# Performance work log

Hardware: AMD Instinct MI355X
Metric: run time of the kernel (lower is better)

The kernel has to match this reference:

```python
import jax, jax.numpy as jnp
import numpy as np

N_NODES = 100000
N_EDGES = 1600000
IN_CH = 128
OUT_CH = 64
HID = 2 * OUT_CH  # 128


def setup_inputs() -> dict:
    key = jax.random.key(0)
    ks = jax.random.split(key, 8)
    s = lambda fan_in: 1.0 / np.sqrt(fan_in)
    return {
        "x": jax.random.normal(ks[0], (N_NODES, IN_CH), jnp.float32),
        "edge_index": jax.random.randint(ks[1], (2, N_EDGES), 0, N_NODES, dtype=jnp.int32),
        "W1": jax.random.normal(ks[2], (IN_CH, HID), jnp.float32) * s(IN_CH),
        "b1": jnp.zeros((HID,), jnp.float32),
        "W2": jax.random.normal(ks[3], (HID, HID), jnp.float32) * s(HID),
        "b2": jnp.zeros((HID,), jnp.float32),
        "W3": jax.random.normal(ks[4], (HID, OUT_CH), jnp.float32) * s(HID),
        "b3": jnp.zeros((OUT_CH,), jnp.float32),
    }


def reference(x, edge_index, W1, b1, W2, b2, W3, b3):
    N = x.shape[0]
    # GCNConv (PyG semantics): add self-loops, symmetric deg^{-1/2} normalization,
    # linear transform, scatter-add aggregation at destination, then bias.
    loops = jnp.arange(N, dtype=edge_index.dtype)
    src = jnp.concatenate([edge_index[0], loops])  # [E+N]
    dst = jnp.concatenate([edge_index[1], loops])  # [E+N]
    deg = jnp.zeros((N,), x.dtype).at[dst].add(1.0)  # in-degree incl. self-loop
    dinv = jnp.where(deg > 0, jax.lax.rsqrt(deg), 0.0)
    norm = (dinv[src] * dinv[dst])[:, None]  # [E+N, 1]

    def gcn_conv(h, W, b):
        h = h @ W  # transform first (smaller when out < in)
        msg = h[src] * norm  # gather + normalize, [E+N, C]
        agg = jnp.zeros((N, h.shape[1]), h.dtype).at[dst].add(msg)  # scatter-add
        return agg + b

    h = jax.nn.relu(gcn_conv(x, W1, b1))
    h = jax.nn.relu(gcn_conv(h, W2, b2))
    h = gcn_conv(h, W3, b3)
    return jnp.min(h, axis=0)  # min-pool over nodes -> [OUT_CH]
```

## Files before the change

### kernel.cpp

```cpp
#include <hip/hip_runtime.h>
#include <stdint.h>
#include <stddef.h>
#include <float.h>

typedef short bf16x8 __attribute__((ext_vector_type(8)));
typedef float f32x4 __attribute__((ext_vector_type(4)));

static __device__ __forceinline__ unsigned enc_min(float v) {
  unsigned u = __float_as_uint(v);
  return (u & 0x80000000u) ? ~u : (u | 0x80000000u);
}
static __device__ __forceinline__ unsigned short f2bf(float f) {
  unsigned u = __float_as_uint(f);
  u += 0x7fffu + ((u >> 16) & 1u);
  return (unsigned short)(u >> 16);
}
static __device__ __forceinline__ float bf2f(unsigned short b) {
  return __uint_as_float(((unsigned)b) << 16);
}
static __device__ __forceinline__ void acc8(float* a, uint4 v) {
  a[0] += __uint_as_float(v.x << 16);
  a[1] += __uint_as_float(v.x & 0xffff0000u);
  a[2] += __uint_as_float(v.y << 16);
  a[3] += __uint_as_float(v.y & 0xffff0000u);
  a[4] += __uint_as_float(v.z << 16);
  a[5] += __uint_as_float(v.z & 0xffff0000u);
  a[6] += __uint_as_float(v.w << 16);
  a[7] += __uint_as_float(v.w & 0xffff0000u);
}

__global__ __launch_bounds__(256) void k_count_bin(const int* __restrict__ edge, int E, int N,
                                                   int* __restrict__ cnt8,
                                                   int* __restrict__ bin_cur,
                                                   int2* __restrict__ pairs,
                                                   int binw, int bcap) {
  __shared__ int h[8], gbase[8], lfill[8];
  int cslot = blockIdx.x & 7;
  int* cnt = cnt8 + (size_t)cslot * N;
  int tid = threadIdx.x;
  int nt = (E + 1023) >> 10;
  for (int t = blockIdx.x; t < nt; t += gridDim.x) {
    int e0 = t << 10;
    if (tid < 8) { h[tid] = 0; lfill[tid] = 0; }
    __syncthreads();
    int d[4], s[4], g[4], r[4];
#pragma unroll
    for (int k = 0; k < 4; ++k) {
      int e = e0 + tid + k * 256;
      d[k] = -1;
      if (e < E) {
        d[k] = edge[E + e];
        s[k] = edge[e];
        g[k] = (int)((unsigned)d[k] / (unsigned)binw);
        r[k] = atomicAdd(&cnt[d[k]], 1);
        atomicAdd(&h[g[k]], 1);
      }
    }
    __syncthreads();
    if (tid < 8) gbase[tid] = atomicAdd(&bin_cur[tid], h[tid]);
    __syncthreads();
#pragma unroll
    for (int k = 0; k < 4; ++k) {
      if (d[k] >= 0) {
        int rr = atomicAdd(&lfill[g[k]], 1);
        int p = gbase[g[k]] + rr;
        unsigned packed = (unsigned)d[k] | ((unsigned)cslot << 17) | ((unsigned)r[k] << 20);
        if (p < bcap) pairs[(size_t)g[k] * bcap + p] = make_int2((int)packed, s[k]);
      }
    }
    __syncthreads();
  }
}

__global__ void k_scan1(const int* __restrict__ cnt8, int N,
                        int* __restrict__ cnt, int* __restrict__ incl,
                        int* __restrict__ bsum) {
  __shared__ int sm[1024];
  int tid = threadIdx.x;
  int i = blockIdx.x * 1024 + tid;
  int v = 0;
  if (i < N) {
#pragma unroll
    for (int g = 0; g < 8; ++g) v += cnt8[(size_t)g * N + i];
    cnt[i] = v;
  }
  sm[tid] = v;
  __syncthreads();
  for (int off = 1; off < 1024; off <<= 1) {
    int t = (tid >= off) ? sm[tid - off] : 0;
    __syncthreads();
    sm[tid] += t;
    __syncthreads();
  }
  if (i < N) incl[i] = sm[tid];
  if (tid == 1023) bsum[blockIdx.x] = sm[1023];
}

__global__ void k_scan2(const int* __restrict__ bsum, int nb, int* __restrict__ boff) {
  __shared__ int sm[128];
  int tid = threadIdx.x;
  int v = (tid < nb) ? bsum[tid] : 0;
  sm[tid] = v;
  __syncthreads();
  for (int off = 1; off < 128; off <<= 1) {
    int t = (tid >= off) ? sm[tid - off] : 0;
    __syncthreads();
    sm[tid] += t;
    __syncthreads();
  }
  if (tid < nb) boff[tid] = sm[tid] - v;
}

__global__ void k_aux(const int* __restrict__ cnt, const int* __restrict__ cnt8,
                      const int* __restrict__ incl, const int* __restrict__ boff,
                      int N, int E, int* __restrict__ row_ptr,
                      int* __restrict__ base8, float* __restrict__ dinv) {
  int i = blockIdx.x * blockDim.x + threadIdx.x;
  if (i < N) {
    int rp = incl[i] - cnt[i] + boff[i >> 10];
    row_ptr[i] = rp;
    dinv[i] = 1.0f / sqrtf((float)(cnt[i] + 1));
    int run = rp;
#pragma unroll
    for (int c = 0; c < 8; ++c) {
      base8[(size_t)c * N + i] = run;
      run += cnt8[(size_t)c * N + i];
    }
  } else if (i == N) {
    row_ptr[N] = E;
  }
}

__global__ void k_prepw(const float* __restrict__ W1, const float* __restrict__ W2,
                        const float* __restrict__ W3,
                        unsigned short* __restrict__ w1h, unsigned short* __restrict__ w1l,
                        unsigned short* __restrict__ w2h, unsigned short* __restrict__ w2l,
                        unsigned short* __restrict__ w3h, unsigned short* __restrict__ w3l) {
  const int K = 128;
  int idx = blockIdx.x * 256 + threadIdx.x;
  const float* W;
  unsigned short *oh, *ol;
  int Nn, base;
  if (idx < 16384) { W = W1; Nn = 128; oh = w1h; ol = w1l; base = idx; }
  else if (idx < 32768) { W = W2; Nn = 128; oh = w2h; ol = w2l; base = idx - 16384; }
  else if (idx < 40960) { W = W3; Nn = 64; oh = w3h; ol = w3l; base = idx - 32768; }
  else return;
  int n = base / K, k = base % K;
  float w = W[(size_t)k * Nn + n];
  unsigned short h = f2bf(w);
  unsigned short l = f2bf(w - bf2f(h));
  int nf = n >> 4, mloc = n & 15, kci = k >> 5, quad = (k >> 3) & 3, j = k & 7;
  size_t o = ((size_t)((nf * 4 + kci) * 64 + quad * 16 + mloc)) * 8 + j;
  oh[o] = h;
  ol[o] = l;
}

template <int NFW>
static __device__ __forceinline__ void gemm_body(const float* __restrict__ A,
                                                 const unsigned short* __restrict__ Wfh,
                                                 const unsigned short* __restrict__ Wfl,
                                                 const float* __restrict__ dinv,
                                                 unsigned short* __restrict__ P, int M,
                                                 int blk) {
  const int K = 128;
  const int COUT = NFW * 64;
  __shared__ unsigned short Ah[64][136];
  __shared__ unsigned short Al[64][136];
  int tid = threadIdx.x;
  int m0 = blk * 64;
  int w = tid >> 6, lane = tid & 63;

  bf16x8 bh[NFW][4], bl[NFW][4];
#pragma unroll
  for (int i = 0; i < NFW; ++i)
#pragma unroll
    for (int kci = 0; kci < 4; ++kci) {
      size_t o = ((size_t)(((w * NFW + i) * 4 + kci) * 64 + lane)) * 8;
      bh[i][kci] = *(const bf16x8*)&Wfh[o];
      bl[i][kci] = *(const bf16x8*)&Wfl[o];
    }

#pragma unroll
  for (int q = 0; q < 8; ++q) {
    int f = q * 256 + tid;
    int m = f >> 5, k4 = f & 31;
    int row = m0 + m;
    if (row >= M) row = M - 1;
    float4 v = *(const float4*)&A[(size_t)row * K + k4 * 4];
    unsigned short h0 = f2bf(v.x), h1 = f2bf(v.y), h2 = f2bf(v.z), h3 = f2bf(v.w);
    unsigned short l0 = f2bf(v.x - bf2f(h0)), l1 = f2bf(v.y - bf2f(h1));
    unsigned short l2 = f2bf(v.z - bf2f(h2)), l3 = f2bf(v.w - bf2f(h3));
    uint2 hh, ll;
    hh.x = (unsigned)h0 | ((unsigned)h1 << 16);
    hh.y = (unsigned)h2 | ((unsigned)h3 << 16);
    ll.x = (unsigned)l0 | ((unsigned)l1 << 16);
    ll.y = (unsigned)l2 | ((unsigned)l3 << 16);
    *(uint2*)&Ah[m][k4 * 4] = hh;
    *(uint2*)&Al[m][k4 * 4] = ll;
  }
  __syncthreads();

  int mloc = lane & 15, quad = lane >> 4;
  f32x4 acc[4][NFW];
#pragma unroll
  for (int rt = 0; rt < 4; ++rt)
#pragma unroll
    for (int i = 0; i < NFW; ++i) acc[rt][i] = (f32x4){0.f, 0.f, 0.f, 0.f};

#pragma unroll
  for (int rt = 0; rt < 4; ++rt) {
    const unsigned short* ph = &Ah[rt * 16 + mloc][quad * 8];
    const unsigned short* pl = &Al[rt * 16 + mloc][quad * 8];
#pragma unroll
    for (int kci = 0; kci < 4; ++kci) {
      bf16x8 ah = *(const bf16x8*)(ph + kci * 32);
      bf16x8 al = *(const bf16x8*)(pl + kci * 32);
#pragma unroll
      for (int i = 0; i < NFW; ++i) {
        acc[rt][i] = __builtin_amdgcn_mfma_f32_16x16x32_bf16(al, bh[i][kci], acc[rt][i], 0, 0, 0);
        acc[rt][i] = __builtin_amdgcn_mfma_f32_16x16x32_bf16(ah, bl[i][kci], acc[rt][i], 0, 0, 0);
        acc[rt][i] = __builtin_amdgcn_mfma_f32_16x16x32_bf16(ah, bh[i][kci], acc[rt][i], 0, 0, 0);
      }
    }
  }

#pragma unroll
  for (int rt = 0; rt < 4; ++rt) {
    int rbase = m0 + rt * 16 + quad * 4;
#pragma unroll
    for (int r = 0; r < 4; ++r) {
      int row = rbase + r;
      if (row < M) {
        float dv = dinv[row];
#pragma unroll
        for (int i = 0; i < NFW; ++i) {
          int nf = w * NFW + i;
          P[(size_t)row * COUT + nf * 16 + mloc] = f2bf(acc[rt][i][r] * dv);
        }
      }
    }
  }
}

__global__ __launch_bounds__(256) void k_fill_gemm(const float* __restrict__ A,
                                                   const unsigned short* __restrict__ Wfh,
                                                   const unsigned short* __restrict__ Wfl,
                                                   const float* __restrict__ dinv,
                                                   unsigned short* __restrict__ P, int M,
                                                   const int2* __restrict__ pairs,
                                                   const int* __restrict__ bin_cur, int bcap,
                                                   const int* __restrict__ base8, int N,
                                                   int* __restrict__ srcs, int ns) {
  if ((int)blockIdx.x >= ns) {
    gemm_body<2>(A, Wfh, Wfl, dinv, P, M, blockIdx.x - ns);
  } else {
    int grp = blockIdx.x & 7;
    int bslot = blockIdx.x >> 3;
    int nslot = ns >> 3;
    int cnt_g = bin_cur[grp];
    if (cnt_g > bcap) cnt_g = bcap;
    const int2* pp = pairs + (size_t)grp * bcap;
    for (int i = bslot * blockDim.x + threadIdx.x; i < cnt_g; i += nslot * blockDim.x) {
      int2 pr = pp[i];
      unsigned w = (unsigned)pr.x;
      int d = (int)(w & 0x1FFFFu);
      int c = (int)((w >> 17) & 7u);
      int r = (int)(w >> 20);
      srcs[base8[(size_t)c * N + d] + r] = pr.y;
    }
  }
}

template <int NFW>
__global__ __launch_bounds__(256) void k_agg_gemm(const unsigned short* __restrict__ Pin,
                                                  const int* __restrict__ row_ptr,
                                                  const int* __restrict__ srcs,
                                                  const float* __restrict__ dinv,
                                                  const float* __restrict__ bias,
                                                  const unsigned short* __restrict__ Wfh,
                                                  const unsigned short* __restrict__ Wfl,
                                                  unsigned short* __restrict__ Pout, int N) {
  const int COUT = NFW * 64;
  __shared__ unsigned short Ah[16][136];
  __shared__ unsigned short Al[16][136];
  int tid = threadIdx.x;
  int wv = tid >> 6, lane = tid & 63;
  int grp = lane >> 4, sub = lane & 15;
  int m = wv * 4 + grp;
  int d = blockIdx.x * 16 + m;
  int dc = d < N ? d : N - 1;
  bool valid = d < N;
  unsigned soff = (unsigned)sub * 16u;
  const char* Pb = (const char*)Pin;

  float a[8] = {0.f, 0.f, 0.f, 0.f, 0.f, 0.f, 0.f, 0.f};
  {
    uint4 v = *(const uint4*)(Pb + ((unsigned)dc * 256u + soff));
    acc8(a, v);
  }
  int lo = row_ptr[dc];
  int hi = row_ptr[valid ? d + 1 : dc];
  int j = lo;
  for (; j + 8 <= hi; j += 8) {
    unsigned id[8];
    uint4 vv[8];
#pragma unroll
    for (int k = 0; k < 8; ++k) id[k] = (unsigned)srcs[j + k];
#pragma unroll
    for (int k = 0; k < 8; ++k) vv[k] = *(const uint4*)(Pb + (id[k] * 256u + soff));
#pragma unroll
    for (int k = 0; k < 8; ++k) acc8(a, vv[k]);
  }
  for (; j + 4 <= hi; j += 4) {
    unsigned id[4];
    uint4 vv[4];
#pragma unroll
    for (int k = 0; k < 4; ++k) id[k] = (unsigned)srcs[j + k];
#pragma unroll
    for (int k = 0; k < 4; ++k) vv[k] = *(const uint4*)(Pb + (id[k] * 256u + soff));
#pragma unroll
    for (int k = 0; k < 4; ++k) acc8(a, vv[k]);
  }
  for (; j < hi; ++j) {
    unsigned i0 = (unsigned)srcs[j];
    uint4 v0 = *(const uint4*)(Pb + (i0 * 256u + soff));
    acc8(a, v0);
  }

  bf16x8 bh[NFW][4], bl[NFW][4];
#pragma unroll
  for (int i = 0; i < NFW; ++i)
#pragma unroll
    for (int kci = 0; kci < 4; ++kci) {
      size_t o = ((size_t)(((wv * NFW + i) * 4 + kci) * 64 + lane)) * 8;
      bh[i][kci] = *(const bf16x8*)&Wfh[o];
      bl[i][kci] = *(const bf16x8*)&Wfl[o];
    }

  float dv = dinv[dc];
  int ch0 = sub * 8;
  float4 bv0 = *(const float4*)&bias[ch0];
  float4 bv1 = *(const float4*)&bias[ch0 + 4];
  float h[8];
  h[0] = dv * a[0] + bv0.x; h[1] = dv * a[1] + bv0.y;
  h[2] = dv * a[2] + bv0.z; h[3] = dv * a[3] + bv0.w;
  h[4] = dv * a[4] + bv1.x; h[5] = dv * a[5] + bv1.y;
  h[6] = dv * a[6] + bv1.z; h[7] = dv * a[7] + bv1.w;
#pragma unroll
  for (int k = 0; k < 8; ++k) h[k] = fmaxf(h[k], 0.f);
  unsigned short hb[8], lb[8];
#pragma unroll
  for (int k = 0; k < 8; ++k) {
    hb[k] = f2bf(h[k]);
    lb[k] = f2bf(h[k] - bf2f(hb[k]));
  }
  uint4 HH, LL;
  HH.x = (unsigned)hb[0] | ((unsigned)hb[1] << 16);
  HH.y = (unsigned)hb[2] | ((unsigned)hb[3] << 16);
  HH.z = (unsigned)hb[4] | ((unsigned)hb[5] << 16);
  HH.w = (unsigned)hb[6] | ((unsigned)hb[7] << 16);
  LL.x = (unsigned)lb[0] | ((unsigned)lb[1] << 16);
  LL.y = (unsigned)lb[2] | ((unsigned)lb[3] << 16);
  LL.z = (unsigned)lb[4] | ((unsigned)lb[5] << 16);
  LL.w = (unsigned)lb[6] | ((unsigned)lb[7] << 16);
  *(uint4*)&Ah[m][ch0] = HH;
  *(uint4*)&Al[m][ch0] = LL;
  __syncthreads();

  int mloc = lane & 15, quad = lane >> 4;
  f32x4 acc[NFW];
#pragma unroll
  for (int i = 0; i < NFW; ++i) acc[i] = (f32x4){0.f, 0.f, 0.f, 0.f};
#pragma unroll
  for (int kci = 0; kci < 4; ++kci) {
    bf16x8 ah = *(const bf16x8*)&Ah[mloc][quad * 8 + kci * 32];
    bf16x8 al = *(const bf16x8*)&Al[mloc][quad * 8 + kci * 32];
#pragma unroll
    for (int i = 0; i < NFW; ++i) {
      acc[i] = __builtin_amdgcn_mfma_f32_16x16x32_bf16(al, bh[i][kci], acc[i], 0, 0, 0);
      acc[i] = __builtin_amdgcn_mfma_f32_16x16x32_bf16(ah, bl[i][kci], acc[i], 0, 0, 0);
      acc[i] = __builtin_amdgcn_mfma_f32_16x16x32_bf16(ah, bh[i][kci], acc[i], 0, 0, 0);
    }
  }
  int rbase = blockIdx.x * 16 + quad * 4;
#pragma unroll
  for (int r = 0; r < 4; ++r) {
    int row = rbase + r;
    if (row < N) {
      float dvr = dinv[row];
#pragma unroll
      for (int i = 0; i < NFW; ++i) {
        int nf = wv * NFW + i;
        Pout[(size_t)row * COUT + nf * 16 + mloc] = f2bf(acc[i][r] * dvr);
      }
    }
  }
}

__global__ __launch_bounds__(256) void k_agg_pool(const unsigned short* __restrict__ P,
                                                  const int* __restrict__ row_ptr,
                                                  const int* __restrict__ srcs,
                                                  const float* __restrict__ dinv,
                                                  const float* __restrict__ bias,
                                                  unsigned* __restrict__ minenc, int N) {
  __shared__ float s_red[4][64];
  int tid = threadIdx.x;
  int wv = tid >> 6, lane = tid & 63;
  int g = lane >> 3, q = lane & 7;
  int d = blockIdx.x * 32 + wv * 8 + g;
  bool valid = d < N;
  int dc = valid ? d : N - 1;
  const char* Pb = (const char*)P;
  unsigned soff = (unsigned)q * 16u;

  float a[8] = {0.f, 0.f, 0.f, 0.f, 0.f, 0.f, 0.f, 0.f};
  {
    uint4 v = *(const uint4*)(Pb + ((unsigned)dc * 128u + soff));
    acc8(a, v);
  }
  int lo = row_ptr[dc];
  int hi = row_ptr[valid ? d + 1 : dc];
  int j = lo;
  for (; j + 8 <= hi; j += 8) {
    unsigned id[8];
    uint4 vv[8];
#pragma unroll
    for (int k = 0; k < 8; ++k) id[k] = (unsigned)srcs[j + k];
#pragma unroll
    for (int k = 0; k < 8; ++k) vv[k] = *(const uint4*)(Pb + (id[k] * 128u + soff));
#pragma unroll
    for (int k = 0; k < 8; ++k) acc8(a, vv[k]);
  }
  for (; j < hi; ++j) {
    unsigned i0 = (unsigned)srcs[j];
    uint4 v0 = *(const uint4*)(Pb + (i0 * 128u + soff));
    acc8(a, v0);
  }

  float dv = dinv[dc];
  int c0 = q * 8;
  float4 bv0 = *(const float4*)&bias[c0];
  float4 bv1 = *(const float4*)&bias[c0 + 4];
  float h[8];
  h[0] = dv * a[0] + bv0.x; h[1] = dv * a[1] + bv0.y;
  h[2] = dv * a[2] + bv0.z; h[3] = dv * a[3] + bv0.w;
  h[4] = dv * a[4] + bv1.x; h[5] = dv * a[5] + bv1.y;
  h[6] = dv * a[6] + bv1.z; h[7] = dv * a[7] + bv1.w;
  if (!valid) {
#pragma unroll
    for (int k = 0; k < 8; ++k) h[k] = FLT_MAX;
  }
#pragma unroll
  for (int off = 8; off < 64; off <<= 1) {
#pragma unroll
    for (int k = 0; k < 8; ++k) h[k] = fminf(h[k], __shfl_xor(h[k], off, 64));
  }
  if (lane < 8) {
#pragma unroll
    for (int k = 0; k < 8; ++k) s_red[wv][q * 8 + k] = h[k];
  }
  __syncthreads();
  if (tid < 64) {
    float mn = fminf(fminf(s_red[0][tid], s_red[1][tid]),
                     fminf(s_red[2][tid], s_red[3][tid]));
    atomicMin(&minenc[tid], enc_min(mn));
  }
}

__global__ void k_decode(const unsigned* __restrict__ minenc, float* __restrict__ out) {
  int c = threadIdx.x;
  unsigned k = minenc[c];
  unsigned u = (k & 0x80000000u) ? (k & 0x7FFFFFFFu) : ~k;
  out[c] = __uint_as_float(u);
}

extern "C" void kernel_launch(void* const* d_in, const int* in_sizes, int n_in,
                              void* d_out, int out_size, void* d_ws, size_t ws_size,
                              hipStream_t stream) {
  const float* X  = (const float*)d_in[0];
  const int* edge = (const int*)d_in[1];
  const float* W1 = (const float*)d_in[2];
  const float* b1 = (const float*)d_in[3];
  const float* W2 = (const float*)d_in[4];
  const float* b2 = (const float*)d_in[5];
  const float* W3 = (const float*)d_in[6];
  const float* b3 = (const float*)d_in[7];
  float* out = (float*)d_out;

  const int IN_CH = 128;
  int N = in_sizes[0] / IN_CH;
  int E = in_sizes[1] / 2;

  char* ws = (char*)d_ws;
  size_t off = 0;
  auto alloc = [&](size_t bytes) {
    void* p = ws + off;
    off = (off + bytes + 255) & ~(size_t)255;
    return p;
  };
  unsigned short* P1 = (unsigned short*)alloc((size_t)N * 128 * 2);
  unsigned short* P2 = (unsigned short*)alloc((size_t)N * 128 * 2);
  int* srcs      = (int*)alloc((size_t)E * 4);
  int* cnt8      = (int*)alloc((size_t)8 * N * 4);
  int* base8     = (int*)alloc((size_t)8 * N * 4);
  int* cnt       = (int*)alloc((size_t)N * 4);
  int* incl      = (int*)alloc((size_t)N * 4);
  int* row_ptr   = (int*)alloc((size_t)(N + 1) * 4);
  float* dinv    = (float*)alloc((size_t)N * 4);
  int* bsum      = (int*)alloc(1024);
  int* boff      = (int*)alloc(1024);
  int* bin_cur   = (int*)alloc(256);
  unsigned* minenc = (unsigned*)alloc(256);
  unsigned short* w1h = (unsigned short*)alloc(16384 * 2);
  unsigned short* w1l = (unsigned short*)alloc(16384 * 2);
  unsigned short* w2h = (unsigned short*)alloc(16384 * 2);
  unsigned short* w2l = (unsigned short*)alloc(16384 * 2);
  unsigned short* w3h = (unsigned short*)alloc(8192 * 2);
  unsigned short* w3l = (unsigned short*)alloc(8192 * 2);

  int bcap = E / 8 + 65536;
  int binw = (N + 7) / 8;
  int2* pairs = (int2*)P2;
  unsigned short* P3 = P1;

  hipMemsetAsync(cnt8, 0, (size_t)8 * N * 4, stream);
  hipMemsetAsync(bin_cur, 0, 32, stream);
  hipMemsetAsync(minenc, 0xFF, 64 * 4, stream);

  int nb = (N + 1023) / 1024;
  int gx = (N + 63) / 64;
  int ns = 1024;
  int gagg = (N + 15) / 16;
  int gpool = (N + 31) / 32;
  k_prepw<<<160, 256, 0, stream>>>(W1, W2, W3, w1h, w1l, w2h, w2l, w3h, w3l);
  k_count_bin<<<782, 256, 0, stream>>>(edge, E, N, cnt8, bin_cur, pairs, binw, bcap);
  k_scan1<<<nb, 1024, 0, stream>>>(cnt8, N, cnt, incl, bsum);
  k_scan2<<<1, 128, 0, stream>>>(bsum, nb, boff);
  k_aux<<<(N + 256) / 256, 256, 0, stream>>>(cnt, cnt8, incl, boff, N, E, row_ptr, base8, dinv);

  k_fill_gemm<<<ns + gx, 256, 0, stream>>>(X, w1h, w1l, dinv, P1, N,
                                           pairs, bin_cur, bcap, base8, N, srcs, ns);
  k_agg_gemm<2><<<gagg, 256, 0, stream>>>(P1, row_ptr, srcs, dinv, b1, w2h, w2l, P2, N);
  k_agg_gemm<1><<<gagg, 256, 0, stream>>>(P2, row_ptr, srcs, dinv, b2, w3h, w3l, P3, N);
  k_agg_pool<<<gpool, 256, 0, stream>>>(P3, row_ptr, srcs, dinv, b3, minenc, N);
  k_decode<<<1, 64, 0, stream>>>(minenc, out);
}
```

Before: 435.9 us.

## Overlap first-layer GEMM with edge counting, defer dinv scaling to scatter kernel

The first-layer GEMM moves from the scatter/fill kernel into the edge-counting kernel, so the matmul runs concurrently with the degree/binning pass. Because dinv is not yet known at that point, the GEMM writes unscaled fp32 results to a new temporary buffer. Extra blocks in the scatter kernel then apply dinv and convert to bf16. This adds a 51MB fp32 write plus a read-back to gain that overlap.

```diff
diff --git a/kernel.cpp b/kernel.cpp
--- a/kernel.cpp
+++ b/kernel.cpp
@@ -27,108 +27,6 @@
   a[5] += __uint_as_float(v.z & 0xffff0000u);
   a[6] += __uint_as_float(v.w << 16);
   a[7] += __uint_as_float(v.w & 0xffff0000u);
-}
-
-__global__ __launch_bounds__(256) void k_count_bin(const int* __restrict__ edge, int E, int N,
-                                                   int* __restrict__ cnt8,
-                                                   int* __restrict__ bin_cur,
-                                                   int2* __restrict__ pairs,
-                                                   int binw, int bcap) {
-  __shared__ int h[8], gbase[8], lfill[8];
-  int cslot = blockIdx.x & 7;
-  int* cnt = cnt8 + (size_t)cslot * N;
-  int tid = threadIdx.x;
-  int nt = (E + 1023) >> 10;
-  for (int t = blockIdx.x; t < nt; t += gridDim.x) {
-    int e0 = t << 10;
-    if (tid < 8) { h[tid] = 0; lfill[tid] = 0; }
-    __syncthreads();
-    int d[4], s[4], g[4], r[4];
-#pragma unroll
-    for (int k = 0; k < 4; ++k) {
-      int e = e0 + tid + k * 256;
-      d[k] = -1;
-      if (e < E) {
-        d[k] = edge[E + e];
-        s[k] = edge[e];
-        g[k] = (int)((unsigned)d[k] / (unsigned)binw);
-        r[k] = atomicAdd(&cnt[d[k]], 1);
-        atomicAdd(&h[g[k]], 1);
-      }
-    }
-    __syncthreads();
-    if (tid < 8) gbase[tid] = atomicAdd(&bin_cur[tid], h[tid]);
-    __syncthreads();
-#pragma unroll
-    for (int k = 0; k < 4; ++k) {
-      if (d[k] >= 0) {
-        int rr = atomicAdd(&lfill[g[k]], 1);
-        int p = gbase[g[k]] + rr;
-        unsigned packed = (unsigned)d[k] | ((unsigned)cslot << 17) | ((unsigned)r[k] << 20);
-        if (p < bcap) pairs[(size_t)g[k] * bcap + p] = make_int2((int)packed, s[k]);
-      }
-    }
-    __syncthreads();
-  }
-}
-
-__global__ void k_scan1(const int* __restrict__ cnt8, int N,
-                        int* __restrict__ cnt, int* __restrict__ incl,
-                        int* __restrict__ bsum) {
-  __shared__ int sm[1024];
-  int tid = threadIdx.x;
-  int i = blockIdx.x * 1024 + tid;
-  int v = 0;
-  if (i < N) {
-#pragma unroll
-    for (int g = 0; g < 8; ++g) v += cnt8[(size_t)g * N + i];
-    cnt[i] = v;
-  }
-  sm[tid] = v;
-  __syncthreads();
-  for (int off = 1; off < 1024; off <<= 1) {
-    int t = (tid >= off) ? sm[tid - off] : 0;
-    __syncthreads();
-    sm[tid] += t;
-    __syncthreads();
-  }
-  if (i < N) incl[i] = sm[tid];
-  if (tid == 1023) bsum[blockIdx.x] = sm[1023];
-}
-
-__global__ void k_scan2(const int* __restrict__ bsum, int nb, int* __restrict__ boff) {
-  __shared__ int sm[128];
-  int tid = threadIdx.x;
-  int v = (tid < nb) ? bsum[tid] : 0;
-  sm[tid] = v;
-  __syncthreads();
-  for (int off = 1; off < 128; off <<= 1) {
-    int t = (tid >= off) ? sm[tid - off] : 0;
-    __syncthreads();
-    sm[tid] += t;
-    __syncthreads();
-  }
-  if (tid < nb) boff[tid] = sm[tid] - v;
-}
-
-__global__ void k_aux(const int* __restrict__ cnt, const int* __restrict__ cnt8,
-                      const int* __restrict__ incl, const int* __restrict__ boff,
-                      int N, int E, int* __restrict__ row_ptr,
-                      int* __restrict__ base8, float* __restrict__ dinv) {
-  int i = blockIdx.x * blockDim.x + threadIdx.x;
-  if (i < N) {
-    int rp = incl[i] - cnt[i] + boff[i >> 10];
-    row_ptr[i] = rp;
-    dinv[i] = 1.0f / sqrtf((float)(cnt[i] + 1));
-    int run = rp;
-#pragma unroll
-    for (int c = 0; c < 8; ++c) {
-      base8[(size_t)c * N + i] = run;
-      run += cnt8[(size_t)c * N + i];
-    }
-  } else if (i == N) {
-    row_ptr[N] = E;
-  }
 }
 
 __global__ void k_prepw(const float* __restrict__ W1, const float* __restrict__ W2,
@@ -155,15 +53,13 @@
   ol[o] = l;
 }
 
-template <int NFW>
-static __device__ __forceinline__ void gemm_body(const float* __restrict__ A,
-                                                 const unsigned short* __restrict__ Wfh,
-                                                 const unsigned short* __restrict__ Wfl,
-                                                 const float* __restrict__ dinv,
-                                                 unsigned short* __restrict__ P, int M,
-                                                 int blk) {
+static __device__ __forceinline__ void gemm1_body_f32(const float* __restrict__ A,
+                                                      const unsigned short* __restrict__ Wfh,
+                                                      const unsigned short* __restrict__ Wfl,
+                                                      float* __restrict__ Ptmp, int M,
+                                                      int blk) {
   const int K = 128;
-  const int COUT = NFW * 64;
+  const int NFW = 2;
   __shared__ unsigned short Ah[64][136];
   __shared__ unsigned short Al[64][136];
   int tid = threadIdx.x;
@@ -231,29 +127,137 @@
     for (int r = 0; r < 4; ++r) {
       int row = rbase + r;
       if (row < M) {
-        float dv = dinv[row];
 #pragma unroll
         for (int i = 0; i < NFW; ++i) {
           int nf = w * NFW + i;
-          P[(size_t)row * COUT + nf * 16 + mloc] = f2bf(acc[rt][i][r] * dv);
+          __builtin_nontemporal_store(acc[rt][i][r],
+                                      &Ptmp[(size_t)row * 128 + nf * 16 + mloc]);
         }
       }
     }
   }
 }
 
-__global__ __launch_bounds__(256) void k_fill_gemm(const float* __restrict__ A,
-                                                   const unsigned short* __restrict__ Wfh,
-                                                   const unsigned short* __restrict__ Wfl,
-                                                   const float* __restrict__ dinv,
-                                                   unsigned short* __restrict__ P, int M,
-                                                   const int2* __restrict__ pairs,
-                                                   const int* __restrict__ bin_cur, int bcap,
-                                                   const int* __restrict__ base8, int N,
-                                                   int* __restrict__ srcs, int ns) {
-  if ((int)blockIdx.x >= ns) {
-    gemm_body<2>(A, Wfh, Wfl, dinv, P, M, blockIdx.x - ns);
-  } else {
+__global__ __launch_bounds__(256) void k_count_gemm(const int* __restrict__ edge, int E, int N,
+                                                    int* __restrict__ cnt8,
+                                                    int* __restrict__ bin_cur,
+                                                    int2* __restrict__ pairs,
+                                                    int binw, int bcap,
+                                                    const float* __restrict__ X,
+                                                    const unsigned short* __restrict__ w1h,
+                                                    const unsigned short* __restrict__ w1l,
+                                                    float* __restrict__ Ptmp,
+                                                    int ncb) {
+  if ((int)blockIdx.x >= ncb) {
+    gemm1_body_f32(X, w1h, w1l, Ptmp, N, blockIdx.x - ncb);
+    return;
+  }
+  __shared__ int h[8], gbase[8], lfill[8];
+  int cslot = blockIdx.x & 7;
+  int* cnt = cnt8 + (size_t)cslot * N;
+  int tid = threadIdx.x;
+  int nt = (E + 1023) >> 10;
+  for (int t = blockIdx.x; t < nt; t += ncb) {
+    int e0 = t << 10;
+    if (tid < 8) { h[tid] = 0; lfill[tid] = 0; }
+    __syncthreads();
+    int d[4], s[4], g[4], r[4];
+#pragma unroll
+    for (int k = 0; k < 4; ++k) {
+      int e = e0 + tid + k * 256;
+      d[k] = -1;
+      if (e < E) {
+        d[k] = edge[E + e];
+        s[k] = edge[e];
+        g[k] = (int)((unsigned)d[k] / (unsigned)binw);
+        r[k] = atomicAdd(&cnt[d[k]], 1);
+        atomicAdd(&h[g[k]], 1);
+      }
+    }
+    __syncthreads();
+    if (tid < 8) gbase[tid] = atomicAdd(&bin_cur[tid], h[tid]);
+    __syncthreads();
+#pragma unroll
+    for (int k = 0; k < 4; ++k) {
+      if (d[k] >= 0) {
+        int rr = atomicAdd(&lfill[g[k]], 1);
+        int p = gbase[g[k]] + rr;
+        unsigned packed = (unsigned)d[k] | ((unsigned)cslot << 17) | ((unsigned)r[k] << 20);
+        if (p < bcap) pairs[(size_t)g[k] * bcap + p] = make_int2((int)packed, s[k]);
+      }
+    }
+    __syncthreads();
+  }
+}
+
+__global__ void k_scan1(const int* __restrict__ cnt8, int N,
+                        int* __restrict__ cnt, int* __restrict__ incl,
+                        int* __restrict__ bsum) {
+  __shared__ int sm[1024];
+  int tid = threadIdx.x;
+  int i = blockIdx.x * 1024 + tid;
+  int v = 0;
+  if (i < N) {
+#pragma unroll
+    for (int g = 0; g < 8; ++g) v += cnt8[(size_t)g * N + i];
+    cnt[i] = v;
+  }
+  sm[tid] = v;
+  __syncthreads();
+  for (int off = 1; off < 1024; off <<= 1) {
+    int t = (tid >= off) ? sm[tid - off] : 0;
+    __syncthreads();
+    sm[tid] += t;
+    __syncthreads();
+  }
+  if (i < N) incl[i] = sm[tid];
+  if (tid == 1023) bsum[blockIdx.x] = sm[1023];
+}
+
+__global__ void k_scan2(const int* __restrict__ bsum, int nb, int* __restrict__ boff) {
+  __shared__ int sm[128];
+  int tid = threadIdx.x;
+  int v = (tid < nb) ? bsum[tid] : 0;
+  sm[tid] = v;
+  __syncthreads();
+  for (int off = 1; off < 128; off <<= 1) {
+    int t = (tid >= off) ? sm[tid - off] : 0;
+    __syncthreads();
+    sm[tid] += t;
+    __syncthreads();
+  }
+  if (tid < nb) boff[tid] = sm[tid] - v;
+}
+
+__global__ void k_aux(const int* __restrict__ cnt, const int* __restrict__ cnt8,
+                      const int* __restrict__ incl, const int* __restrict__ boff,
+                      int N, int E, int* __restrict__ row_ptr,
+                      int* __restrict__ base8, float* __restrict__ dinv) {
+  int i = blockIdx.x * blockDim.x + threadIdx.x;
+  if (i < N) {
+    int rp = incl[i] - cnt[i] + boff[i >> 10];
+    row_ptr[i] = rp;
+    dinv[i] = 1.0f / sqrtf((float)(cnt[i] + 1));
+    int run = rp;
+#pragma unroll
+    for (int c = 0; c < 8; ++c) {
+      base8[(size_t)c * N + i] = run;
+      run += cnt8[(size_t)c * N + i];
+    }
+  } else if (i == N) {
+    row_ptr[N] = E;
+  }
+}
+
+__global__ __launch_bounds__(256) void k_scatter_scale(const int2* __restrict__ pairs,
+                                                       const int* __restrict__ bin_cur, int bcap,
+                                                       const int* __restrict__ base8, int N,
+                                                       int* __restrict__ srcs,
+                                                       const float* __restrict__ Ptmp,
+                                                       const float* __restrict__ dinv,
+                                                       unsigned short* __restrict__ P1,
+                                                       int ns) {
+  if ((int)blockIdx.x < ns) {
     int grp = blockIdx.x & 7;
     int bslot = blockIdx.x >> 3;
     int nslot = ns >> 3;
@@ -267,6 +271,17 @@
       int c = (int)((w >> 17) & 7u);
       int r = (int)(w >> 20);
       srcs[base8[(size_t)c * N + d] + r] = pr.y;
+    }
+  } else {
+    int nb2 = gridDim.x - ns;
+    int total = N * 32;
+    for (int i = (blockIdx.x - ns) * 256 + threadIdx.x; i < total; i += nb2 * 256) {
+      float4 v = *(const float4*)&Ptmp[(size_t)i * 4];
+      float dv = dinv[i >> 5];
+      uint2 o;
+      o.x = (unsigned)f2bf(v.x * dv) | ((unsigned)f2bf(v.y * dv) << 16);
+      o.y = (unsigned)f2bf(v.z * dv) | ((unsigned)f2bf(v.w * dv) << 16);
+      *(uint2*)&P1[(size_t)i * 4] = o;
     }
   }
 }
@@ -500,6 +515,7 @@
   };
   unsigned short* P1 = (unsigned short*)alloc((size_t)N * 128 * 2);
   unsigned short* P2 = (unsigned short*)alloc((size_t)N * 128 * 2);
+  float* Ptmp    = (float*)alloc((size_t)N * 128 * 4);
   int* srcs      = (int*)alloc((size_t)E * 4);
   int* cnt8      = (int*)alloc((size_t)8 * N * 4);
   int* base8     = (int*)alloc((size_t)8 * N * 4);
@@ -529,17 +545,19 @@
 
   int nb = (N + 1023) / 1024;
   int gx = (N + 63) / 64;
+  int ncb = 782;
   int ns = 1024;
+  int nsc = 4096;
   int gagg = (N + 15) / 16;
   int gpool = (N + 31) / 32;
   k_prepw<<<160, 256, 0, stream>>>(W1, W2, W3, w1h, w1l, w2h, w2l, w3h, w3l);
-  k_count_bin<<<782, 256, 0, stream>>>(edge, E, N, cnt8, bin_cur, pairs, binw, bcap);
+  k_count_gemm<<<ncb + gx, 256, 0, stream>>>(edge, E, N, cnt8, bin_cur, pairs, binw, bcap,
+                                             X, w1h, w1l, Ptmp, ncb);
   k_scan1<<<nb, 1024, 0, stream>>>(cnt8, N, cnt, incl, bsum);
   k_scan2<<<1, 128, 0, stream>>>(bsum, nb, boff);
   k_aux<<<(N + 256) / 256, 256, 0, stream>>>(cnt, cnt8, incl, boff, N, E, row_ptr, base8, dinv);
-
-  k_fill_gemm<<<ns + gx, 256, 0, stream>>>(X, w1h, w1l, dinv, P1, N,
-                                           pairs, bin_cur, bcap, base8, N, srcs, ns);
+  k_scatter_scale<<<ns + nsc, 256, 0, stream>>>(pairs, bin_cur, bcap, base8, N, srcs,
+                                                Ptmp, dinv, P1, ns);
   k_agg_gemm<2><<<gagg, 256, 0, stream>>>(P1, row_ptr, srcs, dinv, b1, w2h, w2l, P2, N);
   k_agg_gemm<1><<<gagg, 256, 0, stream>>>(P2, row_ptr, srcs, dinv, b2, w3h, w3l, P3, N);
   k_agg_pool<<<gpool, 256, 0, stream>>>(P3, row_ptr, srcs, dinv, b3, minenc, N);
```

Result: slower. 445.8 us (+2.3%).
